# Performance work log

Measured on AMD Instinct MI355X. Metric: run time of the kernel, lower is better.

Reference implementation:

```python
import jax, jax.numpy as jnp
import numpy as np

N_ENT = 50000
N_EDGE = 500000
D = 256          # ent_hidden_size
H1, C1 = 8, 64   # conv1: heads=8, out=64, concat -> 512
NEG_SLOPE = 0.2
LN_EPS = 1e-5


def setup_inputs() -> dict:
    key = jax.random.key(0)
    ks = jax.random.split(key, 12)
    s = 0.05  # small init scale for numerical sanity
    return {
        "edge_index": jax.random.randint(ks[0], (2, N_EDGE), 0, N_ENT),
        "x": jax.random.normal(ks[1], (N_ENT, D), dtype=jnp.float32),
        "ln_w": jnp.ones((D,), jnp.float32),
        "ln_b": jnp.zeros((D,), jnp.float32),
        "W1": jax.random.normal(ks[2], (D, H1 * C1), dtype=jnp.float32) * s,
        "att_src1": jax.random.normal(ks[3], (H1, C1), dtype=jnp.float32) * s,
        "att_dst1": jax.random.normal(ks[4], (H1, C1), dtype=jnp.float32) * s,
        "b1": jnp.zeros((H1 * C1,), jnp.float32),
        "W2": jax.random.normal(ks[5], (H1 * C1, D), dtype=jnp.float32) * s,
        "att_src2": jax.random.normal(ks[6], (1, D), dtype=jnp.float32) * s,
        "att_dst2": jax.random.normal(ks[7], (1, D), dtype=jnp.float32) * s,
        "b2": jnp.zeros((D,), jnp.float32),
    }


def _gat_conv(x, edge_index, W, att_src, att_dst, bias, heads, out_ch, concat):
    """PyG GATConv (shared src/dst lin, add_self_loops=True, eval-mode dropout)."""
    n = x.shape[0]
    loops = jnp.arange(n)
    src = jnp.concatenate([edge_index[0], loops])  # [E+N]
    dst = jnp.concatenate([edge_index[1], loops])

    h = (x @ W).reshape(n, heads, out_ch)                 # [N,H,C]
    a_src = jnp.sum(h * att_src[None], axis=-1)           # [N,H]
    a_dst = jnp.sum(h * att_dst[None], axis=-1)           # [N,H]

    e = jax.nn.leaky_relu(a_src[src] + a_dst[dst], NEG_SLOPE)  # [E+N,H]
    # per-destination segment softmax (every dst has a self-loop -> no empties)
    m = jax.lax.stop_gradient(jax.ops.segment_max(e, dst, num_segments=n))
    p = jnp.exp(e - m[dst])
    denom = jax.ops.segment_sum(p, dst, num_segments=n)
    alpha = p / denom[dst]                                # [E+N,H]

    out = jax.ops.segment_sum(h[src] * alpha[..., None], dst, num_segments=n)  # [N,H,C]
    out = out.reshape(n, heads * out_ch) if concat else out.mean(axis=1)
    return out + bias


def reference(edge_index, x, ln_w, ln_b, W1, att_src1, att_dst1, b1,
              W2, att_src2, att_dst2, b2):
    # LayerNorm(ent_hidden), eps=1e-5; dropouts are eval-mode no-ops
    mu = jnp.mean(x, axis=-1, keepdims=True)
    var = jnp.var(x, axis=-1, keepdims=True)
    h = (x - mu) / jnp.sqrt(var + LN_EPS) * ln_w + ln_b
    h = jax.nn.elu(_gat_conv(h, edge_index, W1, att_src1, att_dst1, b1, H1, C1, True))
    return _gat_conv(h, edge_index, W2, att_src2, att_dst2, b2, 1, D, False)
```

## Files before the change

### kernel.cpp

```cpp
#include <hip/hip_runtime.h>
#include <hip/hip_bf16.h>
#include <cstdint>

#define N_ENT  50000
#define N_EDGE 500000
#define D_IN   256
constexpr int ETOT = N_EDGE + N_ENT;

typedef __attribute__((ext_vector_type(8))) short bfrag;
typedef __attribute__((ext_vector_type(4))) float f4acc;

__device__ __forceinline__ float lrelu(float x) { return x > 0.f ? x : 0.2f * x; }
__device__ __forceinline__ float eluf(float x)  { return x > 0.f ? x : (expf(x) - 1.f); }
__device__ __forceinline__ short to_bf16(float f) {
    __hip_bfloat16 b = __float2bfloat16(f);
    return *(short*)&b;
}
__device__ __forceinline__ float2 bf2_to_f32(unsigned int u) {
    float2 r;
    r.x = __uint_as_float(u << 16);
    r.y = __uint_as_float(u & 0xffff0000u);
    return r;
}

__global__ __launch_bounds__(256) void ln_kernel(const float* __restrict__ x,
        const float* __restrict__ w, const float* __restrict__ b,
        short* __restrict__ y)
{
    int n = blockIdx.x * 4 + (threadIdx.x >> 6);
    int lane = threadIdx.x & 63;
    const float4 v = *(const float4*)(x + (size_t)n * D_IN + lane * 4);
    float s  = v.x + v.y + v.z + v.w;
    float sq = v.x*v.x + v.y*v.y + v.z*v.z + v.w*v.w;
    #pragma unroll
    for (int off = 1; off < 64; off <<= 1) {
        s  += __shfl_xor(s, off);
        sq += __shfl_xor(sq, off);
    }
    float mean = s * (1.f / 256.f);
    float var  = sq * (1.f / 256.f) - mean * mean;
    float rstd = rsqrtf(var + 1e-5f);
    float4 wv = *(const float4*)(w + lane * 4);
    float4 bv = *(const float4*)(b + lane * 4);
    short4 o;
    o.x = to_bf16((v.x - mean) * rstd * wv.x + bv.x);
    o.y = to_bf16((v.y - mean) * rstd * wv.y + bv.y);
    o.z = to_bf16((v.z - mean) * rstd * wv.z + bv.z);
    o.w = to_bf16((v.w - mean) * rstd * wv.w + bv.w);
    *(short4*)(y + (size_t)n * D_IN + lane * 4) = o;
}

__global__ __launch_bounds__(256) void transpose_bf16_kernel(const float* __restrict__ W,
        short* __restrict__ WT, int R, int C)
{
    int i = blockIdx.x * 256 + threadIdx.x;
    if (i >= R * C) return;
    int r = i / C, c = i - r * C;
    WT[c * R + r] = to_bf16(W[i]);
}

template<int NN, int KK>
__global__ __launch_bounds__(256) void gemm_mfma(const short* __restrict__ A,
        const short* __restrict__ BT, short* __restrict__ C, int M)
{
    __shared__ short As[128 * 32];
    __shared__ short Bs[128 * 32];
    const int tid  = threadIdx.x;
    const int w    = tid >> 6;
    const int l    = tid & 63;
    const int wm   = w >> 1, wn = w & 1;
    const int m0   = blockIdx.y * 128;
    const int n0   = blockIdx.x * 128;
    const int quad = l >> 4;
    const int ln16 = l & 15;
    const int rl   = l >> 2;
    const int cs   = l & 3;

    f4acc acc[4][4];
    #pragma unroll
    for (int i = 0; i < 4; ++i)
        #pragma unroll
        for (int j = 0; j < 4; ++j)
            acc[i][j] = (f4acc){0.f, 0.f, 0.f, 0.f};

    for (int k0 = 0; k0 < KK; k0 += 32) {
        __syncthreads();
        #pragma unroll
        for (int tt = 0; tt < 2; ++tt) {
            int t   = w * 2 + tt;
            int row = t * 16 + rl;
            int ca  = cs ^ ((row >> 1) & 3);
            const short* ga = A + (size_t)(m0 + row) * KK + k0 + ca * 8;
            __builtin_amdgcn_global_load_lds(
                (const __attribute__((address_space(1))) unsigned int*)ga,
                (__attribute__((address_space(3))) unsigned int*)&As[t * 512], 16, 0, 0);
            const short* gb = BT + (size_t)(n0 + row) * KK + k0 + ca * 8;
            __builtin_amdgcn_global_load_lds(
                (const __attribute__((address_space(1))) unsigned int*)gb,
                (__attribute__((address_space(3))) unsigned int*)&Bs[t * 512], 16, 0, 0);
        }
        __syncthreads();
        bfrag af[4], bf[4];
        #pragma unroll
        for (int i = 0; i < 4; ++i) {
            int r = wm * 64 + i * 16 + ln16;
            af[i] = *(const bfrag*)&As[r * 32 + (quad ^ ((r >> 1) & 3)) * 8];
            int rn = wn * 64 + i * 16 + ln16;
            bf[i] = *(const bfrag*)&Bs[rn * 32 + (quad ^ ((rn >> 1) & 3)) * 8];
        }
        #pragma unroll
        for (int i = 0; i < 4; ++i)
            #pragma unroll
            for (int j = 0; j < 4; ++j)
                acc[i][j] = __builtin_amdgcn_mfma_f32_16x16x32_bf16(af[i], bf[j], acc[i][j], 0, 0, 0);
    }
    #pragma unroll
    for (int i = 0; i < 4; ++i) {
        #pragma unroll
        for (int p = 0; p < 4; ++p) {
            int gr = m0 + wm * 64 + i * 16 + quad * 4 + p;
            if (gr < M) {
                #pragma unroll
                for (int j = 0; j < 4; ++j) {
                    int gc = n0 + wn * 64 + j * 16 + ln16;
                    C[(size_t)gr * NN + gc] = to_bf16(acc[i][j][p]);
                }
            }
        }
    }
}

template<int H, int C>
__global__ __launch_bounds__(256) void attn_dots_kernel(const short* __restrict__ feat,
        const float* __restrict__ att_s, const float* __restrict__ att_d,
        float* __restrict__ a_s, float* __restrict__ a_d, int N)
{
    constexpr int F = H * C;
    constexpr int PL = F / 64;
    int n = blockIdx.x * 4 + (threadIdx.x >> 6);
    if (n >= N) return;
    int lane = threadIdx.x & 63;
    int f0 = lane * PL;
    int h = f0 / C;
    float fv[PL];
    const unsigned int* fp = (const unsigned int*)(feat + (size_t)n * F + f0);
    #pragma unroll
    for (int j = 0; j < PL / 2; ++j) {
        float2 t = bf2_to_f32(fp[j]);
        fv[2 * j] = t.x; fv[2 * j + 1] = t.y;
    }
    float ps = 0.f, pd = 0.f;
    #pragma unroll
    for (int j = 0; j < PL; ++j) {
        ps = fmaf(fv[j], att_s[f0 + j], ps);
        pd = fmaf(fv[j], att_d[f0 + j], pd);
    }
    constexpr int GROUP = 64 / H;
    #pragma unroll
    for (int off = 1; off < GROUP; off <<= 1) {
        ps += __shfl_xor(ps, off);
        pd += __shfl_xor(pd, off);
    }
    if ((lane & (GROUP - 1)) == 0) {
        a_s[(size_t)n * H + h] = ps;
        a_d[(size_t)n * H + h] = pd;
    }
}

__global__ __launch_bounds__(256) void count_kernel(const int* __restrict__ ei,
        int* __restrict__ cnt)
{
    int e = blockIdx.x * 256 + threadIdx.x;
    if (e < N_EDGE) atomicAdd(&cnt[ei[N_EDGE + e]], 1);
}

__global__ __launch_bounds__(256) void alloc_kernel(const int* __restrict__ cnt,
        int* __restrict__ row_start, int* __restrict__ cursor)
{
    int d = blockIdx.x * 256 + threadIdx.x;
    int lane = threadIdx.x & 63;
    int c = (d < N_ENT) ? cnt[d] : 0;
    int inc = c;
    #pragma unroll
    for (int off = 1; off < 64; off <<= 1) {
        int nb = __shfl_up(inc, off);
        if (lane >= off) inc += nb;
    }
    int waveTotal = __shfl(inc, 63);
    int base = 0;
    if (lane == 63) base = atomicAdd(cursor, waveTotal);
    base = __shfl(base, 63);
    if (d < N_ENT) row_start[d] = base + inc - c;
}

__global__ __launch_bounds__(256) void fill_csr_kernel(const int* __restrict__ ei,
        const int* __restrict__ row_start, int* __restrict__ cursor2,
        int* __restrict__ csr_src)
{
    int e = blockIdx.x * 256 + threadIdx.x;
    if (e >= N_EDGE) return;
    int d = ei[N_EDGE + e];
    int pos = atomicAdd(&cursor2[d], 1);
    csr_src[row_start[d] + pos] = ei[e];
}

__global__ __launch_bounds__(256) void aggr1_kernel(const int* __restrict__ csr_src,
        const int* __restrict__ row_start, const int* __restrict__ cnt,
        const short* __restrict__ feat, const float* __restrict__ a_s,
        const float* __restrict__ a_d, const float* __restrict__ bias,
        short* __restrict__ out)
{
    int d = blockIdx.x * 4 + (threadIdx.x >> 6);
    if (d >= N_ENT) return;
    int lane = threadIdx.x & 63;
    int f0 = lane * 8;
    int h = lane >> 3;
    int rs = row_start[d];
    int n = cnt[d];
    float adh = a_d[d * 8 + h];

    float den = 0.f;
    float acc[8] = {0.f, 0.f, 0.f, 0.f, 0.f, 0.f, 0.f, 0.f};
    {
        float p = expf(lrelu(a_s[d * 8 + h] + adh));
        den += p;
        uint4 rv = *(const uint4*)(feat + (size_t)d * 512 + f0);
        float2 t0 = bf2_to_f32(rv.x), t1 = bf2_to_f32(rv.y);
        float2 t2 = bf2_to_f32(rv.z), t3 = bf2_to_f32(rv.w);
        acc[0] += p * t0.x; acc[1] += p * t0.y; acc[2] += p * t1.x; acc[3] += p * t1.y;
        acc[4] += p * t2.x; acc[5] += p * t2.y; acc[6] += p * t3.x; acc[7] += p * t3.y;
    }
    int i = 0;
    for (; i + 4 <= n; i += 4) {
        int s0 = csr_src[rs + i + 0];
        int s1 = csr_src[rs + i + 1];
        int s2 = csr_src[rs + i + 2];
        int s3 = csr_src[rs + i + 3];
        float e0 = a_s[s0 * 8 + h], e1 = a_s[s1 * 8 + h];
        float e2 = a_s[s2 * 8 + h], e3 = a_s[s3 * 8 + h];
        uint4 rv0 = *(const uint4*)(feat + (size_t)s0 * 512 + f0);
        uint4 rv1 = *(const uint4*)(feat + (size_t)s1 * 512 + f0);
        uint4 rv2 = *(const uint4*)(feat + (size_t)s2 * 512 + f0);
        uint4 rv3 = *(const uint4*)(feat + (size_t)s3 * 512 + f0);
        float p0 = expf(lrelu(e0 + adh));
        float p1 = expf(lrelu(e1 + adh));
        float p2 = expf(lrelu(e2 + adh));
        float p3 = expf(lrelu(e3 + adh));
        den += (p0 + p1) + (p2 + p3);
        float2 t0, t1, t2, t3;
        t0 = bf2_to_f32(rv0.x); t1 = bf2_to_f32(rv0.y); t2 = bf2_to_f32(rv0.z); t3 = bf2_to_f32(rv0.w);
        acc[0] += p0 * t0.x; acc[1] += p0 * t0.y; acc[2] += p0 * t1.x; acc[3] += p0 * t1.y;
        acc[4] += p0 * t2.x; acc[5] += p0 * t2.y; acc[6] += p0 * t3.x; acc[7] += p0 * t3.y;
        t0 = bf2_to_f32(rv1.x); t1 = bf2_to_f32(rv1.y); t2 = bf2_to_f32(rv1.z); t3 = bf2_to_f32(rv1.w);
        acc[0] += p1 * t0.x; acc[1] += p1 * t0.y; acc[2] += p1 * t1.x; acc[3] += p1 * t1.y;
        acc[4] += p1 * t2.x; acc[5] += p1 * t2.y; acc[6] += p1 * t3.x; acc[7] += p1 * t3.y;
        t0 = bf2_to_f32(rv2.x); t1 = bf2_to_f32(rv2.y); t2 = bf2_to_f32(rv2.z); t3 = bf2_to_f32(rv2.w);
        acc[0] += p2 * t0.x; acc[1] += p2 * t0.y; acc[2] += p2 * t1.x; acc[3] += p2 * t1.y;
        acc[4] += p2 * t2.x; acc[5] += p2 * t2.y; acc[6] += p2 * t3.x; acc[7] += p2 * t3.y;
        t0 = bf2_to_f32(rv3.x); t1 = bf2_to_f32(rv3.y); t2 = bf2_to_f32(rv3.z); t3 = bf2_to_f32(rv3.w);
        acc[0] += p3 * t0.x; acc[1] += p3 * t0.y; acc[2] += p3 * t1.x; acc[3] += p3 * t1.y;
        acc[4] += p3 * t2.x; acc[5] += p3 * t2.y; acc[6] += p3 * t3.x; acc[7] += p3 * t3.y;
    }
    for (; i < n; ++i) {
        int s = csr_src[rs + i];
        float p = expf(lrelu(a_s[s * 8 + h] + adh));
        den += p;
        uint4 rv = *(const uint4*)(feat + (size_t)s * 512 + f0);
        float2 t0 = bf2_to_f32(rv.x), t1 = bf2_to_f32(rv.y);
        float2 t2 = bf2_to_f32(rv.z), t3 = bf2_to_f32(rv.w);
        acc[0] += p * t0.x; acc[1] += p * t0.y; acc[2] += p * t1.x; acc[3] += p * t1.y;
        acc[4] += p * t2.x; acc[5] += p * t2.y; acc[6] += p * t3.x; acc[7] += p * t3.y;
    }
    float inv = 1.f / den;
    float4 b0 = *(const float4*)(bias + f0);
    float4 b1 = *(const float4*)(bias + f0 + 4);
    short* op = out + (size_t)d * 512 + f0;
    short4 o0, o1;
    o0.x = to_bf16(eluf(acc[0] * inv + b0.x)); o0.y = to_bf16(eluf(acc[1] * inv + b0.y));
    o0.z = to_bf16(eluf(acc[2] * inv + b0.z)); o0.w = to_bf16(eluf(acc[3] * inv + b0.w));
    o1.x = to_bf16(eluf(acc[4] * inv + b1.x)); o1.y = to_bf16(eluf(acc[5] * inv + b1.y));
    o1.z = to_bf16(eluf(acc[6] * inv + b1.z)); o1.w = to_bf16(eluf(acc[7] * inv + b1.w));
    *(short4*)(op) = o0;
    *(short4*)(op + 4) = o1;
}

__global__ __launch_bounds__(256) void aggr2_kernel(const int* __restrict__ csr_src,
        const int* __restrict__ row_start, const int* __restrict__ cnt,
        const short* __restrict__ feat, const float* __restrict__ a_s,
        const float* __restrict__ a_d, const float* __restrict__ bias,
        float* __restrict__ out)
{
    int d = blockIdx.x * 4 + (threadIdx.x >> 6);
    if (d >= N_ENT) return;
    int lane = threadIdx.x & 63;
    int f0 = lane * 4;
    int rs = row_start[d];
    int n = cnt[d];
    float adh = a_d[d];

    float den = 0.f;
    float4 acc = make_float4(0.f, 0.f, 0.f, 0.f);
    {
        float p = expf(lrelu(a_s[d] + adh));
        den += p;
        uint2 rv = *(const uint2*)(feat + (size_t)d * 256 + f0);
        float2 t0 = bf2_to_f32(rv.x), t1 = bf2_to_f32(rv.y);
        acc.x += p * t0.x; acc.y += p * t0.y; acc.z += p * t1.x; acc.w += p * t1.y;
    }
    int i = 0;
    for (; i + 4 <= n; i += 4) {
        int s0 = csr_src[rs + i + 0];
        int s1 = csr_src[rs + i + 1];
        int s2 = csr_src[rs + i + 2];
        int s3 = csr_src[rs + i + 3];
        float e0 = a_s[s0], e1 = a_s[s1], e2 = a_s[s2], e3 = a_s[s3];
        uint2 rv0 = *(const uint2*)(feat + (size_t)s0 * 256 + f0);
        uint2 rv1 = *(const uint2*)(feat + (size_t)s1 * 256 + f0);
        uint2 rv2 = *(const uint2*)(feat + (size_t)s2 * 256 + f0);
        uint2 rv3 = *(const uint2*)(feat + (size_t)s3 * 256 + f0);
        float p0 = expf(lrelu(e0 + adh));
        float p1 = expf(lrelu(e1 + adh));
        float p2 = expf(lrelu(e2 + adh));
        float p3 = expf(lrelu(e3 + adh));
        den += (p0 + p1) + (p2 + p3);
        float2 t0, t1;
        t0 = bf2_to_f32(rv0.x); t1 = bf2_to_f32(rv0.y);
        acc.x += p0 * t0.x; acc.y += p0 * t0.y; acc.z += p0 * t1.x; acc.w += p0 * t1.y;
        t0 = bf2_to_f32(rv1.x); t1 = bf2_to_f32(rv1.y);
        acc.x += p1 * t0.x; acc.y += p1 * t0.y; acc.z += p1 * t1.x; acc.w += p1 * t1.y;
        t0 = bf2_to_f32(rv2.x); t1 = bf2_to_f32(rv2.y);
        acc.x += p2 * t0.x; acc.y += p2 * t0.y; acc.z += p2 * t1.x; acc.w += p2 * t1.y;
        t0 = bf2_to_f32(rv3.x); t1 = bf2_to_f32(rv3.y);
        acc.x += p3 * t0.x; acc.y += p3 * t0.y; acc.z += p3 * t1.x; acc.w += p3 * t1.y;
    }
    for (; i < n; ++i) {
        int s = csr_src[rs + i];
        float p = expf(lrelu(a_s[s] + adh));
        den += p;
        uint2 rv = *(const uint2*)(feat + (size_t)s * 256 + f0);
        float2 t0 = bf2_to_f32(rv.x), t1 = bf2_to_f32(rv.y);
        acc.x += p * t0.x; acc.y += p * t0.y; acc.z += p * t1.x; acc.w += p * t1.y;
    }
    float inv = 1.f / den;
    float4 bv = *(const float4*)(bias + f0);
    float4 o;
    o.x = acc.x * inv + bv.x; o.y = acc.y * inv + bv.y;
    o.z = acc.z * inv + bv.z; o.w = acc.w * inv + bv.w;
    *(float4*)(out + (size_t)d * 256 + f0) = o;
}

extern "C" void kernel_launch(void* const* d_in, const int* in_sizes, int n_in,
                              void* d_out, int out_size, void* d_ws, size_t ws_size,
                              hipStream_t stream)
{
    const int*   ei     = (const int*)  d_in[0];
    const float* x      = (const float*)d_in[1];
    const float* ln_w   = (const float*)d_in[2];
    const float* ln_b   = (const float*)d_in[3];
    const float* W1     = (const float*)d_in[4];
    const float* att_s1 = (const float*)d_in[5];
    const float* att_d1 = (const float*)d_in[6];
    const float* b1     = (const float*)d_in[7];
    const float* W2     = (const float*)d_in[8];
    const float* att_s2 = (const float*)d_in[9];
    const float* att_d2 = (const float*)d_in[10];
    const float* b2     = (const float*)d_in[11];
    float* out = (float*)d_out;

    short* h0b = (short*)d_ws;
    short* h1b = h0b + 12800000;
    short* h2b = h1b + 25600000;
    short* h3b = h2b + 25600000;
    short* W1T = h3b + 12800000;
    short* W2T = W1T + 131072;
    float* a_s1 = (float*)(W2T + 131072);
    float* a_d1 = a_s1 + 400000;
    float* a_s2 = a_d1 + 400000;
    float* a_d2 = a_s2 + 50000;
    int* cnt       = (int*)(a_d2 + 50000);
    int* row_start = cnt + 50000;
    int* cursor2   = row_start + 50000;
    int* csr_src   = cursor2 + 50000;
    int* cursor    = csr_src + 500000;

    hipMemsetAsync(cnt,     0, 50000 * 4, stream);
    hipMemsetAsync(cursor2, 0, 50000 * 4, stream);
    hipMemsetAsync(cursor,  0, 4, stream);

    count_kernel<<<(N_EDGE + 255) / 256, 256, 0, stream>>>(ei, cnt);
    alloc_kernel<<<(N_ENT + 255) / 256, 256, 0, stream>>>(cnt, row_start, cursor);
    fill_csr_kernel<<<(N_EDGE + 255) / 256, 256, 0, stream>>>(ei, row_start, cursor2, csr_src);

    transpose_bf16_kernel<<<(131072 + 255) / 256, 256, 0, stream>>>(W1, W1T, 256, 512);
    transpose_bf16_kernel<<<(131072 + 255) / 256, 256, 0, stream>>>(W2, W2T, 512, 256);

    ln_kernel<<<12500, 256, 0, stream>>>(x, ln_w, ln_b, h0b);

    gemm_mfma<512, 256><<<dim3(4, 391), 256, 0, stream>>>(h0b, W1T, h1b, N_ENT);
    attn_dots_kernel<8, 64><<<12500, 256, 0, stream>>>(h1b, att_s1, att_d1, a_s1, a_d1, N_ENT);
    aggr1_kernel<<<12500, 256, 0, stream>>>(csr_src, row_start, cnt, h1b, a_s1, a_d1, b1, h2b);

    gemm_mfma<256, 512><<<dim3(2, 391), 256, 0, stream>>>(h2b, W2T, h3b, N_ENT);
    attn_dots_kernel<1, 256><<<12500, 256, 0, stream>>>(h3b, att_s2, att_d2, a_s2, a_d2, N_ENT);
    aggr2_kernel<<<12500, 256, 0, stream>>>(csr_src, row_start, cnt, h3b, a_s2, a_d2, b2, out);
}
```

Measured before the change: 405.4 us.

## Fuse attention dot products into GEMM epilogue and use nontemporal loads/stores

Computes the per-head attention source and destination dot products inside the MFMA GEMM epilogue, reducing across the 16 lanes that share an output row. This removes both attn_dots kernels and their re-read of the bf16 feature matrices. For the second layer, where a head spans several column tiles, partial sums are combined with atomic adds into buffers that are zeroed with extra memsets. It also switches the LayerNorm input load and the aggregation output stores to nontemporal accesses to reduce cache pollution.

```diff
diff --git a/kernel.cpp b/kernel.cpp
--- a/kernel.cpp
+++ b/kernel.cpp
@@ -9,6 +9,8 @@
 
 typedef __attribute__((ext_vector_type(8))) short bfrag;
 typedef __attribute__((ext_vector_type(4))) float f4acc;
+typedef __attribute__((ext_vector_type(4))) float f32x4;
+typedef __attribute__((ext_vector_type(8))) short s16x8;
 
 __device__ __forceinline__ float lrelu(float x) { return x > 0.f ? x : 0.2f * x; }
 __device__ __forceinline__ float eluf(float x)  { return x > 0.f ? x : (expf(x) - 1.f); }
@@ -29,7 +31,7 @@
 {
     int n = blockIdx.x * 4 + (threadIdx.x >> 6);
     int lane = threadIdx.x & 63;
-    const float4 v = *(const float4*)(x + (size_t)n * D_IN + lane * 4);
+    const f32x4 v = __builtin_nontemporal_load((const f32x4*)(x + (size_t)n * D_IN + lane * 4));
     float s  = v.x + v.y + v.z + v.w;
     float sq = v.x*v.x + v.y*v.y + v.z*v.z + v.w*v.w;
     #pragma unroll
@@ -59,9 +61,11 @@
     WT[c * R + r] = to_bf16(W[i]);
 }
 
-template<int NN, int KK>
+template<int NN, int KK, int CH>
 __global__ __launch_bounds__(256) void gemm_mfma(const short* __restrict__ A,
-        const short* __restrict__ BT, short* __restrict__ C, int M)
+        const short* __restrict__ BT, short* __restrict__ C,
+        const float* __restrict__ att_s, const float* __restrict__ att_d,
+        float* __restrict__ a_s, float* __restrict__ a_d, int M)
 {
     __shared__ short As[128 * 32];
     __shared__ short Bs[128 * 32];
@@ -114,56 +118,50 @@
             for (int j = 0; j < 4; ++j)
                 acc[i][j] = __builtin_amdgcn_mfma_f32_16x16x32_bf16(af[i], bf[j], acc[i][j], 0, 0, 0);
     }
+
+    const int hh = (n0 + wn * 64) / CH;
+    float as_c[4], ad_c[4];
+    #pragma unroll
+    for (int j = 0; j < 4; ++j) {
+        int gc = n0 + wn * 64 + j * 16 + ln16;
+        as_c[j] = att_s[gc];
+        ad_c[j] = att_d[gc];
+    }
+
     #pragma unroll
     for (int i = 0; i < 4; ++i) {
         #pragma unroll
         for (int p = 0; p < 4; ++p) {
             int gr = m0 + wm * 64 + i * 16 + quad * 4 + p;
+            float ps = 0.f, pd = 0.f;
+            #pragma unroll
+            for (int j = 0; j < 4; ++j) {
+                float c = acc[i][j][p];
+                ps = fmaf(c, as_c[j], ps);
+                pd = fmaf(c, ad_c[j], pd);
+            }
+            #pragma unroll
+            for (int off = 1; off < 16; off <<= 1) {
+                ps += __shfl_xor(ps, off);
+                pd += __shfl_xor(pd, off);
+            }
             if (gr < M) {
                 #pragma unroll
                 for (int j = 0; j < 4; ++j) {
                     int gc = n0 + wn * 64 + j * 16 + ln16;
                     C[(size_t)gr * NN + gc] = to_bf16(acc[i][j][p]);
                 }
+                if (ln16 == 0) {
+                    if constexpr (CH <= 64) {
+                        a_s[(size_t)gr * (NN / CH) + hh] = ps;
+                        a_d[(size_t)gr * (NN / CH) + hh] = pd;
+                    } else {
+                        unsafeAtomicAdd(&a_s[gr], ps);
+                        unsafeAtomicAdd(&a_d[gr], pd);
+                    }
+                }
             }
         }
-    }
-}
-
-template<int H, int C>
-__global__ __launch_bounds__(256) void attn_dots_kernel(const short* __restrict__ feat,
-        const float* __restrict__ att_s, const float* __restrict__ att_d,
-        float* __restrict__ a_s, float* __restrict__ a_d, int N)
-{
-    constexpr int F = H * C;
-    constexpr int PL = F / 64;
-    int n = blockIdx.x * 4 + (threadIdx.x >> 6);
-    if (n >= N) return;
-    int lane = threadIdx.x & 63;
-    int f0 = lane * PL;
-    int h = f0 / C;
-    float fv[PL];
-    const unsigned int* fp = (const unsigned int*)(feat + (size_t)n * F + f0);
-    #pragma unroll
-    for (int j = 0; j < PL / 2; ++j) {
-        float2 t = bf2_to_f32(fp[j]);
-        fv[2 * j] = t.x; fv[2 * j + 1] = t.y;
-    }
-    float ps = 0.f, pd = 0.f;
-    #pragma unroll
-    for (int j = 0; j < PL; ++j) {
-        ps = fmaf(fv[j], att_s[f0 + j], ps);
-        pd = fmaf(fv[j], att_d[f0 + j], pd);
-    }
-    constexpr int GROUP = 64 / H;
-    #pragma unroll
-    for (int off = 1; off < GROUP; off <<= 1) {
-        ps += __shfl_xor(ps, off);
-        pd += __shfl_xor(pd, off);
-    }
-    if ((lane & (GROUP - 1)) == 0) {
-        a_s[(size_t)n * H + h] = ps;
-        a_d[(size_t)n * H + h] = pd;
     }
 }
 
@@ -274,14 +272,12 @@
     float inv = 1.f / den;
     float4 b0 = *(const float4*)(bias + f0);
     float4 b1 = *(const float4*)(bias + f0 + 4);
-    short* op = out + (size_t)d * 512 + f0;
-    short4 o0, o1;
-    o0.x = to_bf16(eluf(acc[0] * inv + b0.x)); o0.y = to_bf16(eluf(acc[1] * inv + b0.y));
-    o0.z = to_bf16(eluf(acc[2] * inv + b0.z)); o0.w = to_bf16(eluf(acc[3] * inv + b0.w));
-    o1.x = to_bf16(eluf(acc[4] * inv + b1.x)); o1.y = to_bf16(eluf(acc[5] * inv + b1.y));
-    o1.z = to_bf16(eluf(acc[6] * inv + b1.z)); o1.w = to_bf16(eluf(acc[7] * inv + b1.w));
-    *(short4*)(op) = o0;
-    *(short4*)(op + 4) = o1;
+    s16x8 o;
+    o[0] = to_bf16(eluf(acc[0] * inv + b0.x)); o[1] = to_bf16(eluf(acc[1] * inv + b0.y));
+    o[2] = to_bf16(eluf(acc[2] * inv + b0.z)); o[3] = to_bf16(eluf(acc[3] * inv + b0.w));
+    o[4] = to_bf16(eluf(acc[4] * inv + b1.x)); o[5] = to_bf16(eluf(acc[5] * inv + b1.y));
+    o[6] = to_bf16(eluf(acc[6] * inv + b1.z)); o[7] = to_bf16(eluf(acc[7] * inv + b1.w));
+    __builtin_nontemporal_store(o, (s16x8*)(out + (size_t)d * 512 + f0));
 }
 
 __global__ __launch_bounds__(256) void aggr2_kernel(const int* __restrict__ csr_src,
@@ -343,10 +339,10 @@
     }
     float inv = 1.f / den;
     float4 bv = *(const float4*)(bias + f0);
-    float4 o;
+    f32x4 o;
     o.x = acc.x * inv + bv.x; o.y = acc.y * inv + bv.y;
     o.z = acc.z * inv + bv.z; o.w = acc.w * inv + bv.w;
-    *(float4*)(out + (size_t)d * 256 + f0) = o;
+    __builtin_nontemporal_store(o, (f32x4*)(out + (size_t)d * 256 + f0));
 }
 
 extern "C" void kernel_launch(void* const* d_in, const int* in_sizes, int n_in,
@@ -386,6 +382,8 @@
     hipMemsetAsync(cnt,     0, 50000 * 4, stream);
     hipMemsetAsync(cursor2, 0, 50000 * 4, stream);
     hipMemsetAsync(cursor,  0, 4, stream);
+    hipMemsetAsync(a_s2,    0, 50000 * 4, stream);
+    hipMemsetAsync(a_d2,    0, 50000 * 4, stream);
 
     count_kernel<<<(N_EDGE + 255) / 256, 256, 0, stream>>>(ei, cnt);
     alloc_kernel<<<(N_ENT + 255) / 256, 256, 0, stream>>>(cnt, row_start, cursor);
@@ -396,11 +394,11 @@
 
     ln_kernel<<<12500, 256, 0, stream>>>(x, ln_w, ln_b, h0b);
 
-    gemm_mfma<512, 256><<<dim3(4, 391), 256, 0, stream>>>(h0b, W1T, h1b, N_ENT);
-    attn_dots_kernel<8, 64><<<12500, 256, 0, stream>>>(h1b, att_s1, att_d1, a_s1, a_d1, N_ENT);
+    gemm_mfma<512, 256, 64><<<dim3(4, 391), 256, 0, stream>>>(
+        h0b, W1T, h1b, att_s1, att_d1, a_s1, a_d1, N_ENT);
     aggr1_kernel<<<12500, 256, 0, stream>>>(csr_src, row_start, cnt, h1b, a_s1, a_d1, b1, h2b);
 
-    gemm_mfma<256, 512><<<dim3(2, 391), 256, 0, stream>>>(h2b, W2T, h3b, N_ENT);
-    attn_dots_kernel<1, 256><<<12500, 256, 0, stream>>>(h3b, att_s2, att_d2, a_s2, a_d2, N_ENT);
+    gemm_mfma<256, 512, 256><<<dim3(2, 391), 256, 0, stream>>>(
+        h2b, W2T, h3b, att_s2, att_d2, a_s2, a_d2, N_ENT);
     aggr2_kernel<<<12500, 256, 0, stream>>>(csr_src, row_start, cnt, h3b, a_s2, a_d2, b2, out);
 }
```

Measured after the change: 411.3 us. Within noise of the previous version (+1.5%).
